# Performance work log

Measured on AMD Instinct MI355X. Metric: run time of the kernel, lower is better.

## Reference

```python
import jax, jax.numpy as jnp
import numpy as np

B, T, D, H = 2, 2048, 1024, 16
HD = D // H
EPS = 1e-5


def setup_inputs() -> dict:
    key = jax.random.key(0)
    ks = jax.random.split(key, 6)
    scale = 0.02
    return {
        "x": jax.random.normal(ks[0], (B, T, D), dtype=jnp.float32),
        "wq": jax.random.normal(ks[1], (D, D), dtype=jnp.float32) * scale,
        "bq": jnp.zeros((D,), dtype=jnp.float32),
        "wk": jax.random.normal(ks[2], (D, D), dtype=jnp.float32) * scale,
        "bk": jnp.zeros((D,), dtype=jnp.float32),
        "wv": jax.random.normal(ks[3], (D, D), dtype=jnp.float32) * scale,
        "bv": jnp.zeros((D,), dtype=jnp.float32),
        "wg": jax.random.normal(ks[4], (D, D), dtype=jnp.float32) * scale,
        "bg": jnp.zeros((D,), dtype=jnp.float32),
        "gamma": jnp.ones((D,), dtype=jnp.float32),
        "beta": jnp.zeros((D,), dtype=jnp.float32),
    }


def reference(x, wq, bq, wk, bk, wv, bv, wg, bg, gamma, beta):
    b, t, d = x.shape
    # projections (torch Linear: y = x @ W^T + b, W stored as (out, in))
    def proj(w, bias):
        return jnp.einsum('btd,ed->bte', x, w) + bias
    q = proj(wq, bq).reshape(b, t, H, HD).swapaxes(1, 2)  # b h t hd
    k = proj(wk, bk).reshape(b, t, H, HD).swapaxes(1, 2)
    v = proj(wv, bv).reshape(b, t, H, HD).swapaxes(1, 2)
    # full (non-causal) attention as in the source
    scores = jnp.einsum('bhqd,bhkd->bhqk', q, k) / jnp.sqrt(jnp.float32(HD))
    attn = jax.nn.softmax(scores, axis=-1)
    out = jnp.einsum('bhqk,bhkd->bhqd', attn, v)
    out = out.swapaxes(1, 2).reshape(b, t, d)  # b t (h hd)
    gate = proj(wg, bg)
    y = gate * out
    # GroupNorm with n_heads groups over the channel (d_model) dim, per token
    yg = y.reshape(b, t, H, HD)
    mu = jnp.mean(yg, axis=-1, keepdims=True)
    var = jnp.var(yg, axis=-1, keepdims=True)
    yn = (yg - mu) / jnp.sqrt(var + EPS)
    yn = yn * gamma.reshape(H, HD) + beta.reshape(H, HD)
    return yn.reshape(b, t, d)
```

## Files before the change

### kernel.cpp

```cpp
#include <hip/hip_runtime.h>
#include <hip/hip_bf16.h>
#include <math.h>

namespace {
constexpr int kB = 2, kT = 2048, kD = 1024, kH = 16, kHD = 64;
}

typedef __attribute__((ext_vector_type(8))) short short8;
typedef __attribute__((ext_vector_type(4))) float f32x4;
typedef __attribute__((ext_vector_type(16))) float f32x16;

#if __has_builtin(__builtin_amdgcn_exp2f)
#define EXP2F(x) __builtin_amdgcn_exp2f(x)
#else
#define EXP2F(x) __expf((x) * 0.6931471805599453f)
#endif

__device__ __forceinline__ ushort f2bf(float f) {
  union { float f; uint u; } c; c.f = f;
  uint u = c.u + 0x7FFFu + ((c.u >> 16) & 1u);
  return (ushort)(u >> 16);
}

__device__ __forceinline__ float bf2f(ushort u) {
  union { uint u; float f; } c; c.u = ((uint)u) << 16; return c.f;
}

__device__ __forceinline__ uint pack_bf2(float a, float b) {
  uint r;
  asm("v_cvt_pk_bf16_f32 %0, %1, %2" : "=v"(r) : "v"(a), "v"(b));
  return r;
}

__device__ __forceinline__ void gload_lds16(const void* g, void* l) {
  __builtin_amdgcn_global_load_lds(
      (const __attribute__((address_space(1))) void*)g,
      (__attribute__((address_space(3))) void*)l, 16, 0, 0);
}

__global__ __launch_bounds__(256) void cvt_kernel(
    const float* __restrict__ x, const float* __restrict__ w0,
    const float* __restrict__ w1, const float* __restrict__ w2,
    const float* __restrict__ w3, ushort* __restrict__ out)
{
  const size_t g = (size_t)blockIdx.x * 256 + threadIdx.x;
  const size_t e = g * 4;
  const float* src; size_t rel;
  if (e < ((size_t)1 << 22)) { src = x; rel = e; }
  else {
    size_t e2 = e - ((size_t)1 << 22);
    int wi = (int)(e2 >> 20);
    src = wi == 0 ? w0 : wi == 1 ? w1 : wi == 2 ? w2 : w3;
    rel = e2 & (((size_t)1 << 20) - 1);
  }
  float4 v = *reinterpret_cast<const float4*>(src + rel);
  ushort4 u;
  u.x = f2bf(v.x); u.y = f2bf(v.y); u.z = f2bf(v.z); u.w = f2bf(v.w);
  *reinterpret_cast<ushort4*>(out + e) = u;
}

__device__ __forceinline__ void stage_half(
    const ushort* __restrict__ src, int row0, int kcol0,
    ushort* ldsbase, int wid, int lane)
{
#pragma unroll
  for (int part = 0; part < 2; ++part) {
    const int c = part * 512 + wid * 64 + lane;
    const int x = c * 16;
    const int o = x ^ (((x >> 7) & 3) << 4);
    const int r = o >> 6;
    const int cb = (o & 63) >> 1;
    gload_lds16(src + (size_t)(row0 + r) * kD + kcol0 + cb, ldsbase + (x >> 1));
  }
}

__device__ __forceinline__ short8 read_frag(const ushort* half, int r, int lg) {
  const int slot = lg ^ ((r >> 1) & 3);
  return *reinterpret_cast<const short8*>(&half[r * 32 + slot * 8]);
}

#define PH_BAR() do { asm volatile("" ::: "memory"); \
  __builtin_amdgcn_s_barrier(); asm volatile("" ::: "memory"); } while (0)

__global__ __launch_bounds__(512, 2) void proj_mfma_kernel(
    const ushort* __restrict__ Xb, const ushort* __restrict__ Wb,
    const float* __restrict__ bq, const float* __restrict__ bk,
    const float* __restrict__ bv, const float* __restrict__ bg,
    ushort* __restrict__ qo, ushort* __restrict__ ko,
    ushort* __restrict__ vt, ushort* __restrict__ go)
{
  const int mat = blockIdx.z;
  const ushort* Wm = Wb + (size_t)mat * 1024 * 1024;
  const float* bias = mat == 0 ? bq : mat == 1 ? bk : mat == 2 ? bv : bg;
  const int m0 = blockIdx.x * 256;
  const int n0g = blockIdx.y * 256;
  const int tid = threadIdx.x;
  const int wid = tid >> 6, lane = tid & 63;
  const int wr = wid >> 2, wc = wid & 3;
  const int wrow = wr * 128, wcol = wc * 64;
  const int lr = lane & 15, lg = lane >> 4;

  __shared__ ushort lds[65536];

  f32x4 acc[8][4];
#pragma unroll
  for (int i = 0; i < 8; ++i)
#pragma unroll
    for (int j = 0; j < 4; ++j) acc[i][j] = (f32x4){0.f, 0.f, 0.f, 0.f};

  short8 bfr[4];

#define STAGE_A(bu, h, kt) stage_half(Xb, m0,  (kt) * 64 + (h) * 32, \
    &lds[(bu) * 32768 + (h) * 8192], wid, lane)
#define STAGE_B(bu, h, kt) stage_half(Wm, n0g, (kt) * 64 + (h) * 32, \
    &lds[(bu) * 32768 + 16384 + (h) * 8192], wid, lane)

#define PHASE(bu, h, MB, READB, STAGE_STMT, DOVM)                          \
  {                                                                        \
    const ushort* Ah = &lds[(bu) * 32768 + (h) * 8192];                    \
    const ushort* Bh = &lds[(bu) * 32768 + 16384 + (h) * 8192];            \
    short8 af[4];                                                          \
    af[0] = read_frag(Ah, wrow + (MB + 0) * 16 + lr, lg);                  \
    af[1] = read_frag(Ah, wrow + (MB + 1) * 16 + lr, lg);                  \
    af[2] = read_frag(Ah, wrow + (MB + 2) * 16 + lr, lg);                  \
    af[3] = read_frag(Ah, wrow + (MB + 3) * 16 + lr, lg);                  \
    if (READB) {                                                           \
      bfr[0] = read_frag(Bh, wcol + 0 * 16 + lr, lg);                      \
      bfr[1] = read_frag(Bh, wcol + 1 * 16 + lr, lg);                      \
      bfr[2] = read_frag(Bh, wcol + 2 * 16 + lr, lg);                      \
      bfr[3] = read_frag(Bh, wcol + 3 * 16 + lr, lg);                      \
    }                                                                      \
    STAGE_STMT;                                                            \
    PH_BAR();                                                              \
    __builtin_amdgcn_s_setprio(1);                                         \
    _Pragma("unroll")                                                      \
    for (int m2 = 0; m2 < 4; ++m2)                                         \
      _Pragma("unroll")                                                    \
      for (int ni = 0; ni < 4; ++ni)                                       \
        acc[(MB) + m2][ni] = __builtin_amdgcn_mfma_f32_16x16x32_bf16(      \
            af[m2], bfr[ni], acc[(MB) + m2][ni], 0, 0, 0);                 \
    __builtin_amdgcn_s_setprio(0);                                         \
    if (DOVM) asm volatile("s_waitcnt vmcnt(4)" ::: "memory");             \
    PH_BAR();                                                              \
  }

  STAGE_A(0, 0, 0); STAGE_B(0, 0, 0);
  STAGE_A(0, 1, 0); STAGE_B(0, 1, 0);
  STAGE_A(1, 0, 1); STAGE_B(1, 0, 1);
  asm volatile("s_waitcnt vmcnt(4)" ::: "memory");
  PH_BAR();

#pragma unroll 1
  for (int it = 0; it < 8; ++it) {
    const int ta = 2 * it, tb = 2 * it + 1;
    const int tn0 = (ta + 2) & 15;
    const int tn1 = (tb + 2) & 15;
    PHASE(0, 0, 0, 1, (STAGE_A(1, 1, tb)),  0)
    PHASE(0, 0, 4, 0, (STAGE_B(1, 1, tb)),  0)
    PHASE(0, 1, 0, 1, (STAGE_A(0, 0, tn0)), 0)
    PHASE(0, 1, 4, 0, (STAGE_B(0, 0, tn0)), 1)
    PHASE(1, 0, 0, 1, (STAGE_A(0, 1, tn0)), 0)
    PHASE(1, 0, 4, 0, (STAGE_B(0, 1, tn0)), 0)
    PHASE(1, 1, 0, 1, (STAGE_A(1, 0, tn1)), 0)
    PHASE(1, 1, 4, 0, (STAGE_B(1, 0, tn1)), 1)
  }

#undef PHASE
#undef STAGE_A
#undef STAGE_B

  const float vsc = (mat == 0) ? 0.18033688f : 1.0f;

#pragma unroll
  for (int mi = 0; mi < 8; ++mi) {
    const int mbase = m0 + wrow + mi * 16 + 4 * lg;
    const int b = mbase >> 11, t0r = mbase & (kT - 1);
#pragma unroll
    for (int ni = 0; ni < 4; ++ni) {
      const int n = n0g + wcol + ni * 16 + lr;
      const float bn = bias[n];
      if (mat == 3) {
#pragma unroll
        for (int r = 0; r < 4; ++r)
          go[(size_t)(mbase + r) * kD + n] = f2bf(acc[mi][ni][r] + bn);
      } else if (mat == 2) {
        const int h = n >> 6, hd = n & 63;
        const int bh2 = b * kH + h;
        ushort4 u;
        u.x = f2bf(acc[mi][ni][0] + bn); u.y = f2bf(acc[mi][ni][1] + bn);
        u.z = f2bf(acc[mi][ni][2] + bn); u.w = f2bf(acc[mi][ni][3] + bn);
        *reinterpret_cast<ushort4*>(
            &vt[((size_t)bh2 * kHD + hd) * kT + t0r]) = u;
      } else {
        const int h = n >> 6, hd = n & 63;
        const int bh2 = b * kH + h;
        ushort* dst = (mat == 0) ? qo : ko;
#pragma unroll
        for (int r = 0; r < 4; ++r)
          dst[((size_t)bh2 * kT + t0r + r) * kHD + hd] =
              f2bf((acc[mi][ni][r] + bn) * vsc);
      }
    }
  }
}

__global__ __launch_bounds__(256, 4) void attn_mfma32_kernel(
    const ushort* __restrict__ Qrm, const ushort* __restrict__ Krm,
    const ushort* __restrict__ Vtr, ushort* __restrict__ Op,
    float* __restrict__ lsumP)
{
  const int bid = blockIdx.x;
  const int xcd = bid & 7;
  const int j = bid >> 3;
  const int bh = xcd * 4 + (j >> 6);
  const int rem = j & 63;
  const int qt = rem & 15;
  const int ks = rem >> 4;
  const int tid = threadIdx.x, w = tid >> 6, lane = tid & 63;
  const int lq = lane & 31;
  const int hi = lane >> 5;

  __shared__ ushort kvA[4096];
  __shared__ ushort kvB[4096];

  const int q0 = qt * 128 + w * 32;
  short8 aq[4];
#pragma unroll
  for (int hk = 0; hk < 4; ++hk)
    aq[hk] = *reinterpret_cast<const short8*>(
        &Qrm[((size_t)bh * kT + q0 + lq) * kHD + hk * 16 + hi * 8]);

  f32x16 oacc[2];
#pragma unroll
  for (int nh = 0; nh < 2; ++nh)
#pragma unroll
    for (int r = 0; r < 16; ++r) oacc[nh][r] = 0.f;
  float lsum = 0.f;

  const size_t koff = ((size_t)bh * kT + ks * 512 + (tid & 31)) * kHD
                      + (tid >> 6) * 16 + ((tid >> 5) & 1) * 8;
  const size_t voff = ((size_t)bh * kHD + (tid >> 7) * 32 + (tid & 31)) * kT
                      + ks * 512 + ((tid >> 6) & 1) * 16 + ((tid >> 5) & 1) * 8;

#define STAGE_KV(dst, t) do {                                               \
    gload_lds16(Krm + koff + (size_t)(t) * (32 * kHD), &dst[tid * 8]);      \
    gload_lds16(Vtr + voff + (size_t)(t) * 32, &dst[2048 + tid * 8]);       \
  } while (0)

#define COMPUTE_KV(buf) do {                                                \
    short8 kf_[4];                                                          \
    _Pragma("unroll")                                                       \
    for (int hk = 0; hk < 4; ++hk)                                          \
      kf_[hk] = *reinterpret_cast<const short8*>(&buf[(hk * 64 + lane) * 8]);\
    short8 vf[2][2];                                                        \
    _Pragma("unroll")                                                       \
    for (int nh = 0; nh < 2; ++nh)                                          \
      _Pragma("unroll")                                                     \
      for (int jf = 0; jf < 2; ++jf)                                        \
        vf[nh][jf] = *reinterpret_cast<const short8*>(                      \
            &buf[2048 + ((nh * 2 + jf) * 64 + lane) * 8]);                  \
    f32x16 s;                                                               \
    _Pragma("unroll")                                                       \
    for (int r = 0; r < 16; ++r) s[r] = 0.f;                                \
    __builtin_amdgcn_s_setprio(1);                                          \
    _Pragma("unroll")                                                       \
    for (int hk = 0; hk < 4; ++hk)                                          \
      s = __builtin_amdgcn_mfma_f32_32x32x16_bf16(kf_[hk], aq[hk], s, 0, 0, 0);\
    __builtin_amdgcn_s_setprio(0);                                          \
    float p[16];                                                            \
    _Pragma("unroll")                                                       \
    for (int r = 0; r < 16; ++r) p[r] = EXP2F(s[r]);                        \
    float t0 = 0.f, t1 = 0.f;                                               \
    _Pragma("unroll")                                                       \
    for (int r = 0; r < 16; r += 2) { t0 += p[r]; t1 += p[r + 1]; }         \
    lsum += t0 + t1;                                                        \
    uint pk[8];                                                             \
    _Pragma("unroll")                                                       \
    for (int m = 0; m < 8; ++m) pk[m] = pack_bf2(p[2 * m], p[2 * m + 1]);   \
    union { uint u[4]; short8 s8; } fa0, fa1;                               \
    {                                                                       \
      auto s0 = __builtin_amdgcn_permlane32_swap(pk[0], pk[2], false, false);\
      auto s1 = __builtin_amdgcn_permlane32_swap(pk[1], pk[3], false, false);\
      auto s2 = __builtin_amdgcn_permlane32_swap(pk[4], pk[6], false, false);\
      auto s3 = __builtin_amdgcn_permlane32_swap(pk[5], pk[7], false, false);\
      fa0.u[0] = s0[0]; fa0.u[2] = s0[1];                                   \
      fa0.u[1] = s1[0]; fa0.u[3] = s1[1];                                   \
      fa1.u[0] = s2[0]; fa1.u[2] = s2[1];                                   \
      fa1.u[1] = s3[0]; fa1.u[3] = s3[1];                                   \
    }                                                                       \
    __builtin_amdgcn_s_setprio(1);                                          \
    oacc[0] = __builtin_amdgcn_mfma_f32_32x32x16_bf16(vf[0][0], fa0.s8, oacc[0], 0, 0, 0);\
    oacc[0] = __builtin_amdgcn_mfma_f32_32x32x16_bf16(vf[0][1], fa1.s8, oacc[0], 0, 0, 0);\
    oacc[1] = __builtin_amdgcn_mfma_f32_32x32x16_bf16(vf[1][0], fa0.s8, oacc[1], 0, 0, 0);\
    oacc[1] = __builtin_amdgcn_mfma_f32_32x32x16_bf16(vf[1][1], fa1.s8, oacc[1], 0, 0, 0);\
    __builtin_amdgcn_s_setprio(0);                                          \
  } while (0)

  STAGE_KV(kvA, 0);
  __syncthreads();

#pragma unroll 1
  for (int kt = 0; kt < 16; kt += 2) {
    if (kt + 1 < 16) STAGE_KV(kvB, kt + 1);
    COMPUTE_KV(kvA);
    __syncthreads();
    if (kt + 2 < 16) STAGE_KV(kvA, kt + 2);
    COMPUTE_KV(kvB);
    __syncthreads();
  }

#undef STAGE_KV
#undef COMPUTE_KV

  lsum += __shfl_xor(lsum, 32);

  const size_t prow = (((size_t)ks * 32 + bh) * kT + (q0 + lq)) * kHD;
#pragma unroll
  for (int nh = 0; nh < 2; ++nh)
#pragma unroll
    for (int g2 = 0; g2 < 4; ++g2) {
      ushort4 u;
      u.x = f2bf(oacc[nh][4 * g2 + 0]);
      u.y = f2bf(oacc[nh][4 * g2 + 1]);
      u.z = f2bf(oacc[nh][4 * g2 + 2]);
      u.w = f2bf(oacc[nh][4 * g2 + 3]);
      *reinterpret_cast<ushort4*>(&Op[prow + nh * 32 + 8 * g2 + 4 * hi]) = u;
    }
  if (hi == 0)
    lsumP[((size_t)ks * 32 + bh) * kT + q0 + lq] = lsum;
}

__global__ __launch_bounds__(256) void gn_kernel(
    const ushort* __restrict__ gb, const ushort* __restrict__ Op,
    const float* __restrict__ lsumP,
    const float* __restrict__ gamma, const float* __restrict__ beta,
    float* __restrict__ out)
{
  const int tid = threadIdx.x;
  const int grp = blockIdx.x * 16 + (tid >> 4);
  const int l16 = tid & 15;
  const int bt = grp >> 4, h = grp & 15;
  const int b = bt >> 11, t = bt & (kT - 1);
  const int bh = b * kH + h;
  const int c0 = l16 * 4;

  float l = 0.f;
  float ov[4] = {0.f, 0.f, 0.f, 0.f};
#pragma unroll
  for (int ks = 0; ks < 4; ++ks) {
    const size_t base = ((size_t)ks * 32 + bh) * kT + t;
    ushort4 o4 = *reinterpret_cast<const ushort4*>(&Op[base * kHD + c0]);
    ov[0] += bf2f(o4.x); ov[1] += bf2f(o4.y);
    ov[2] += bf2f(o4.z); ov[3] += bf2f(o4.w);
    l += lsumP[base];
  }
  const float inv_l = 1.f / l;
  ushort4 g4 = *reinterpret_cast<const ushort4*>(&gb[(size_t)bt * kD + h * kHD + c0]);
  float y[4];
  y[0] = bf2f(g4.x) * ov[0] * inv_l; y[1] = bf2f(g4.y) * ov[1] * inv_l;
  y[2] = bf2f(g4.z) * ov[2] * inv_l; y[3] = bf2f(g4.w) * ov[3] * inv_l;

  float s = y[0] + y[1] + y[2] + y[3];
  float ss = y[0]*y[0] + y[1]*y[1] + y[2]*y[2] + y[3]*y[3];
#pragma unroll
  for (int off = 8; off; off >>= 1) {
    s  += __shfl_xor(s, off);
    ss += __shfl_xor(ss, off);
  }
  const float mean = s * (1.f / 64.f);
  const float var  = ss * (1.f / 64.f) - mean * mean;
  const float inv  = rsqrtf(var + 1e-5f);

  float4 gm = *reinterpret_cast<const float4*>(&gamma[h * kHD + c0]);
  float4 bt4 = *reinterpret_cast<const float4*>(&beta[h * kHD + c0]);
  float4 o;
  o.x = (y[0] - mean) * inv * gm.x + bt4.x;
  o.y = (y[1] - mean) * inv * gm.y + bt4.y;
  o.z = (y[2] - mean) * inv * gm.z + bt4.z;
  o.w = (y[3] - mean) * inv * gm.w + bt4.w;
  *reinterpret_cast<float4*>(&out[(size_t)bt * kD + h * kHD + c0]) = o;
}

extern "C" void kernel_launch(void* const* d_in, const int* in_sizes, int n_in,
                              void* d_out, int out_size, void* d_ws, size_t ws_size,
                              hipStream_t stream) {
  const float* x     = (const float*)d_in[0];
  const float* wq    = (const float*)d_in[1];
  const float* bq    = (const float*)d_in[2];
  const float* wk    = (const float*)d_in[3];
  const float* bk    = (const float*)d_in[4];
  const float* wv    = (const float*)d_in[5];
  const float* bv    = (const float*)d_in[6];
  const float* wg    = (const float*)d_in[7];
  const float* bg    = (const float*)d_in[8];
  const float* gamma = (const float*)d_in[9];
  const float* beta  = (const float*)d_in[10];

  ushort* cb  = (ushort*)d_ws;
  ushort* qb  = cb + (size_t)8388608;
  ushort* kb  = qb + (size_t)4194304;
  ushort* vtb = kb + (size_t)4194304;
  ushort* gb  = vtb + (size_t)4194304;
  ushort* Op  = gb + (size_t)4194304;
  float*  lsumP = (float*)cb;
  float*  out = (float*)d_out;

  const ushort* xb = cb;
  const ushort* wb = cb + (size_t)4194304;

  cvt_kernel<<<8192, 256, 0, stream>>>(x, wq, wk, wv, wg, cb);
  proj_mfma_kernel<<<dim3(16, 4, 4), 512, 0, stream>>>(
      xb, wb, bq, bk, bv, bg, qb, kb, vtb, gb);
  attn_mfma32_kernel<<<2048, 256, 0, stream>>>(qb, kb, vtb, Op, lsumP);
  gn_kernel<<<4096, 256, 0, stream>>>(gb, Op, lsumP, gamma, beta, out);
}
```

Baseline: 111.2 us.

## Store K and V in MFMA fragment-ordered layout for contiguous LDS staging

The projection epilogue now writes K and V into a pre-swizzled layout that matches the per-lane fragment order the attention kernel reads from LDS. Each 32-key chunk is then a contiguous 4 KB block, so the global-to-LDS loads become fully contiguous per thread instead of strided gathers. The cost is scattered, less coalesced stores in the projection epilogue, especially the per-element K writes.

```diff
diff --git a/kernel.cpp b/kernel.cpp
--- a/kernel.cpp
+++ b/kernel.cpp
@@ -37,6 +37,7 @@
       (const __attribute__((address_space(1))) void*)g,
       (__attribute__((address_space(3))) void*)l, 16, 0, 0);
 }
+
 
 __global__ __launch_bounds__(256) void cvt_kernel(
     const float* __restrict__ x, const float* __restrict__ w0,
@@ -186,18 +187,34 @@
       } else if (mat == 2) {
         const int h = n >> 6, hd = n & 63;
         const int bh2 = b * kH + h;
+        const int nh = hd >> 5, lv = hd & 31;
+        const int kc = t0r >> 5, kk0 = t0r & 31;
+        const int jf = kk0 >> 4, hi2 = (kk0 >> 3) & 1, jj0 = kk0 & 7;
+        const int lane2 = lv + hi2 * 32;
+        const size_t off =
+            (((((size_t)bh2 * 64 + kc) * 2 + nh) * 2 + jf) * 64 + lane2) * 8 + jj0;
         ushort4 u;
         u.x = f2bf(acc[mi][ni][0] + bn); u.y = f2bf(acc[mi][ni][1] + bn);
         u.z = f2bf(acc[mi][ni][2] + bn); u.w = f2bf(acc[mi][ni][3] + bn);
-        *reinterpret_cast<ushort4*>(
-            &vt[((size_t)bh2 * kHD + hd) * kT + t0r]) = u;
+        *reinterpret_cast<ushort4*>(&vt[off]) = u;
+      } else if (mat == 1) {
+        const int h = n >> 6, hd = n & 63;
+        const int bh2 = b * kH + h;
+        const int hk = hd >> 4, hi2 = (hd >> 3) & 1, jj = hd & 7;
+#pragma unroll
+        for (int r = 0; r < 4; ++r) {
+          const int t = t0r + r;
+          const int kc = t >> 5, kk = t & 31;
+          const size_t off =
+              ((((size_t)bh2 * 64 + kc) * 4 + hk) * 64 + kk + hi2 * 32) * 8 + jj;
+          ko[off] = f2bf(acc[mi][ni][r] + bn);
+        }
       } else {
         const int h = n >> 6, hd = n & 63;
         const int bh2 = b * kH + h;
-        ushort* dst = (mat == 0) ? qo : ko;
 #pragma unroll
         for (int r = 0; r < 4; ++r)
-          dst[((size_t)bh2 * kT + t0r + r) * kHD + hd] =
+          qo[((size_t)bh2 * kT + t0r + r) * kHD + hd] =
               f2bf((acc[mi][ni][r] + bn) * vsc);
       }
     }
@@ -205,8 +222,8 @@
 }
 
 __global__ __launch_bounds__(256, 4) void attn_mfma32_kernel(
-    const ushort* __restrict__ Qrm, const ushort* __restrict__ Krm,
-    const ushort* __restrict__ Vtr, ushort* __restrict__ Op,
+    const ushort* __restrict__ Qrm, const ushort* __restrict__ Kf,
+    const ushort* __restrict__ Vf, ushort* __restrict__ Op,
     float* __restrict__ lsumP)
 {
   const int bid = blockIdx.x;
@@ -237,14 +254,12 @@
     for (int r = 0; r < 16; ++r) oacc[nh][r] = 0.f;
   float lsum = 0.f;
 
-  const size_t koff = ((size_t)bh * kT + ks * 512 + (tid & 31)) * kHD
-                      + (tid >> 6) * 16 + ((tid >> 5) & 1) * 8;
-  const size_t voff = ((size_t)bh * kHD + (tid >> 7) * 32 + (tid & 31)) * kT
-                      + ks * 512 + ((tid >> 6) & 1) * 16 + ((tid >> 5) & 1) * 8;
+  const ushort* kbase = Kf + ((size_t)bh * 64 + ks * 16) * 2048;
+  const ushort* vbase = Vf + ((size_t)bh * 64 + ks * 16) * 2048;
 
 #define STAGE_KV(dst, t) do {                                               \
-    gload_lds16(Krm + koff + (size_t)(t) * (32 * kHD), &dst[tid * 8]);      \
-    gload_lds16(Vtr + voff + (size_t)(t) * 32, &dst[2048 + tid * 8]);       \
+    gload_lds16(kbase + (size_t)(t) * 2048 + tid * 8, &dst[tid * 8]);       \
+    gload_lds16(vbase + (size_t)(t) * 2048 + tid * 8, &dst[2048 + tid * 8]);\
   } while (0)
 
 #define COMPUTE_KV(buf) do {                                                \
```

Measured after the change: 106.6 us, median of 2. 4.2% less time.
